# Performance work log

Hardware: AMD Instinct MI355X
Metric: run time of the kernel (lower is better)

Reference implementation:

```python
import jax, jax.numpy as jnp
import numpy as np

L, B, D, Di, N, H, P, K, M, V = 4, 8, 2048, 4096, 128, 64, 64, 4, 8, 50288
Cch = Di + 2 * N           # conv channels = 4352
Dout = 2 * Di + 2 * N + H  # in_proj out = 8512
EPS = 1e-5


def _rms(x, w):
    return x * jax.lax.rsqrt(jnp.mean(x * x, axis=-1, keepdims=True) + EPS) * w


def setup_inputs() -> dict:
    key = jax.random.key(0)
    ks = jax.random.split(key, 16)
    s = 0.02
    return {
        "input_ids": jax.random.randint(ks[0], (B, 1), 0, V),
        "emb": jax.random.normal(ks[1], (V, D)) * s,
        "in_proj_w": jax.random.normal(ks[2], (L, D, Dout)) * s,
        "conv_w": jax.random.normal(ks[3], (L, Cch, K)) * s,
        "conv_b": jax.random.normal(ks[4], (L, Cch)) * s,
        "A_log": jax.random.normal(ks[5], (L, H)) * 0.5,
        "dt_bias": jax.random.normal(ks[6], (L, H)) * 0.5,
        "D_param": jax.random.normal(ks[7], (L, H)) * 0.5,
        "mixer_norm_w": jnp.ones((L, Di)),
        "out_proj_w": jax.random.normal(ks[8], (L, Di, D)) * s,
        "layer_norm_w": jnp.ones((L, D)),
        "norm_f_w": jnp.ones((D,)),
        "W_mc": jax.random.normal(ks[9], (L, M + 1)).at[:, -1].set(5.0),
        "conv_state": jax.random.normal(ks[10], (L, B, Cch, K)) * 0.1,
        "ssm_state": jax.random.normal(ks[11], (L, B, H, P, N)) * 0.1,
        "cached_states": jax.random.normal(ks[12], (L, B, M, H, P, N)) * 0.1,
    }


def reference(input_ids, emb, in_proj_w, conv_w, conv_b, A_log, dt_bias, D_param,
              mixer_norm_w, out_proj_w, layer_norm_w, norm_f_w, W_mc,
              conv_state, ssm_state, cached_states):
    ids = input_ids[:, 0]              # (B,)
    res = emb[ids]                     # (B, D) token embedding gather
    for l in range(L):
        xn = _rms(res, layer_norm_w[l])
        zxbcdt = xn @ in_proj_w[l]     # (B, Dout)
        z = zxbcdt[:, :Di]
        xBC = zxbcdt[:, Di:Di + Cch]
        dt = zxbcdt[:, Di + Cch:]
        # circular conv-state shift + depthwise conv over kernel dim
        cs = jnp.concatenate([conv_state[l][:, :, 1:], xBC[:, :, None]], axis=-1)
        xBC = jax.nn.silu(jnp.sum(cs * conv_w[l][None], axis=-1) + conv_b[l])
        x, Bm, Cm = xBC[:, :Di], xBC[:, Di:Di + N], xBC[:, Di + N:]
        dt = jax.nn.softplus(dt + dt_bias[l])                 # (B, H)
        dA = jnp.exp(dt * (-jnp.exp(A_log[l])))               # (B, H)
        x = x.reshape(B, H, P)
        dBx = jnp.einsum('bh,bn,bhp->bhpn', dt, Bm, x)        # (B,H,P,N)
        ssm = ssm_state[l] * dA[:, :, None, None] + dBx       # (B,H,P,N)
        # softmax-weighted fusion of cached segment states + current state
        w = jax.nn.softmax(W_mc[l])                           # (M+1,)
        fused = jnp.einsum('bmhpn,m->bhpn', cached_states[l], w[:-1]) + w[-1] * ssm
        y = jnp.einsum('bhpn,bn->bhp', fused, Cm) + D_param[l][None, :, None] * x
        y = y.reshape(B, Di)
        y = _rms(y * jax.nn.silu(z), mixer_norm_w[l])         # gated RMSNorm
        res = res + y @ out_proj_w[l]
    res = _rms(res, norm_f_w)
    logits = res @ emb.T               # tied lm_head
    return logits[:, None, :]          # (B, 1, V)
```

## Files before the change

### kernel.cpp

```cpp
#include <hip/hip_runtime.h>
#include <hip/hip_bf16.h>
#include <math.h>

#define LN 4
#define B_ 8
#define D_ 2048
#define DI 4096
#define N_ 128
#define H_ 64
#define P_ 64
#define K_ 4
#define M_ 8
#define V_ 50288
#define CCH (DI + 2*N_)
#define DOUT (2*DI + 2*N_ + H_)
#define EPSF 1e-5f
#define KT_IN 32
#define KT_OUT 128

typedef float f32x4 __attribute__((ext_vector_type(4)));

__device__ inline float wave_sum(float v) {
  #pragma unroll
  for (int off = 32; off > 0; off >>= 1) v += __shfl_xor(v, off, 64);
  return v;
}

__device__ inline float fold_reduce8(const float a[8], int lane) {
  float t0[4];
  #pragma unroll
  for (int r = 0; r < 4; ++r) {
    float keep = (lane & 1) ? a[2*r+1] : a[2*r];
    float send = (lane & 1) ? a[2*r]   : a[2*r+1];
    t0[r] = keep + __shfl_xor(send, 1, 64);
  }
  float t1[2];
  #pragma unroll
  for (int r = 0; r < 2; ++r) {
    float keep = (lane & 2) ? t0[2*r+1] : t0[2*r];
    float send = (lane & 2) ? t0[2*r]   : t0[2*r+1];
    t1[r] = keep + __shfl_xor(send, 2, 64);
  }
  float keep = (lane & 4) ? t1[1] : t1[0];
  float send = (lane & 4) ? t1[0] : t1[1];
  float u = keep + __shfl_xor(send, 4, 64);
  u += __shfl_xor(u, 8, 64);
  u += __shfl_xor(u, 16, 64);
  u += __shfl_xor(u, 32, 64);
  return u;
}

__global__ __launch_bounds__(256)
void k_inproj1_first(const int* __restrict__ ids, const float* __restrict__ emb,
                     const float* __restrict__ lnw, const float* __restrict__ W,
                     float* __restrict__ pin) {
  __shared__ float xs[8][64];
  __shared__ float sred[4][8];
  int tid = threadIdx.x, lane = tid & 63, wid = tid >> 6;
  int jt = blockIdx.x % 9, kt = blockIdx.x / 9;
  int k0 = kt * 64;
  float ssq[8];
  #pragma unroll
  for (int r = 0; r < 8; ++r) {
    const float* row = emb + (size_t)ids[r] * D_;
    f32x4 a = *reinterpret_cast<const f32x4*>(row + tid * 8);
    f32x4 c = *reinterpret_cast<const f32x4*>(row + tid * 8 + 4);
    ssq[r] = a[0]*a[0] + a[1]*a[1] + a[2]*a[2] + a[3]*a[3]
           + c[0]*c[0] + c[1]*c[1] + c[2]*c[2] + c[3]*c[3];
  }
  #pragma unroll
  for (int r = 0; r < 8; ++r) {
    float wsum = wave_sum(ssq[r]);
    if (lane == 0) sred[wid][r] = wsum;
  }
  __syncthreads();
  for (int i = tid; i < 8 * 64; i += 256) {
    int r = i >> 6, kk = i & 63;
    const float* row = emb + (size_t)ids[r] * D_;
    float tot = sred[0][r] + sred[1][r] + sred[2][r] + sred[3][r];
    float scale = rsqrtf(tot / (float)D_ + EPSF);
    xs[r][kk] = row[k0 + kk] * scale * lnw[k0 + kk];
  }
  __syncthreads();
  int j = jt * 1024 + tid * 4;
  if (j >= DOUT) return;
  f32x4 acc[8];
  #pragma unroll
  for (int r = 0; r < 8; ++r) acc[r] = (f32x4)0.f;
  const float* Wp = W + (size_t)k0 * DOUT + j;
  for (int kk = 0; kk < 64; ++kk) {
    f32x4 w4 = __builtin_nontemporal_load(
        reinterpret_cast<const f32x4*>(Wp + (size_t)kk * DOUT));
    #pragma unroll
    for (int r = 0; r < 8; ++r) acc[r] += w4 * xs[r][kk];
  }
  #pragma unroll
  for (int r = 0; r < 8; ++r)
    *reinterpret_cast<f32x4*>(&pin[((size_t)kt * 8 + r) * DOUT + j]) = acc[r];
}

__global__ __launch_bounds__(256)
void k_inproj1(const float* __restrict__ res, const float* __restrict__ ssq_in,
               const float* __restrict__ lnw, const float* __restrict__ W,
               float* __restrict__ pin) {
  __shared__ float xs[8][64];
  int tid = threadIdx.x;
  int jt = blockIdx.x % 9, kt = blockIdx.x / 9;
  int k0 = kt * 64;
  for (int i = tid; i < 8 * 64; i += 256) {
    int r = i >> 6, kk = i & 63;
    float scale = rsqrtf(ssq_in[r] / (float)D_ + EPSF);
    xs[r][kk] = res[r * D_ + k0 + kk] * scale * lnw[k0 + kk];
  }
  __syncthreads();
  int j = jt * 1024 + tid * 4;
  if (j >= DOUT) return;
  f32x4 acc[8];
  #pragma unroll
  for (int r = 0; r < 8; ++r) acc[r] = (f32x4)0.f;
  const float* Wp = W + (size_t)k0 * DOUT + j;
  for (int kk = 0; kk < 64; ++kk) {
    f32x4 w4 = __builtin_nontemporal_load(
        reinterpret_cast<const f32x4*>(Wp + (size_t)kk * DOUT));
    #pragma unroll
    for (int r = 0; r < 8; ++r) acc[r] += w4 * xs[r][kk];
  }
  #pragma unroll
  for (int r = 0; r < 8; ++r)
    *reinterpret_cast<f32x4*>(&pin[((size_t)kt * 8 + r) * DOUT + j]) = acc[r];
}

__global__ __launch_bounds__(256)
void k_inproj2_conv(const float* __restrict__ pin, const float* __restrict__ conv_state,
                    const float* __restrict__ conv_w, const float* __restrict__ conv_b,
                    const float* __restrict__ A_log, const float* __restrict__ dt_bias,
                    const float* __restrict__ W_mc,
                    float* __restrict__ zx, float* __restrict__ xbc,
                    float* __restrict__ dts, float* __restrict__ dav,
                    float* __restrict__ wmc) {
  const int TOT4 = B_ * DOUT / 4;
  int t = blockIdx.x * 256 + threadIdx.x;
  if (t >= TOT4) return;
  f32x4 s = (f32x4)0.f;
  const f32x4* p4 = reinterpret_cast<const f32x4*>(pin) + t;
  #pragma unroll 8
  for (int kt = 0; kt < KT_IN; ++kt) s += p4[(size_t)kt * TOT4];
  reinterpret_cast<f32x4*>(zx)[t] = s;
  int c4 = t * 4;
  int b = c4 / DOUT;
  int c = c4 - b * DOUT;
  #pragma unroll
  for (int e = 0; e < 4; ++e) {
    int ce = c + e;
    if (ce >= DI && ce < DI + CCH) {
      int cc = ce - DI;
      f32x4 cs4 = *reinterpret_cast<const f32x4*>(conv_state + ((size_t)b * CCH + cc) * K_);
      f32x4 cw4 = *reinterpret_cast<const f32x4*>(conv_w + (size_t)cc * K_);
      float v = cs4[1] * cw4[0] + cs4[2] * cw4[1] + cs4[3] * cw4[2]
              + s[e] * cw4[3] + conv_b[cc];
      xbc[b * CCH + cc] = v / (1.f + expf(-v));
    } else if (ce >= DI + CCH) {
      int h = ce - DI - CCH;
      float x = s[e] + dt_bias[h];
      float sp = (x > 20.f) ? x : log1pf(expf(x));
      dts[b * 64 + h] = sp;
      dav[b * 64 + h] = expf(-expf(A_log[h]) * sp);
    }
  }
  if (t == 0) {
    float mx = -1e30f;
    for (int i = 0; i < M_ + 1; ++i) mx = fmaxf(mx, W_mc[i]);
    float e2[M_ + 1], sum = 0.f;
    for (int i = 0; i < M_ + 1; ++i) { e2[i] = expf(W_mc[i] - mx); sum += e2[i]; }
    for (int i = 0; i < M_ + 1; ++i) wmc[i] = e2[i] / sum;
  }
}

__global__ __launch_bounds__(256)
void k_state(const float* __restrict__ xbc, const float* __restrict__ dts,
             const float* __restrict__ dav, const float* __restrict__ Dp_,
             const float* __restrict__ wmc, const float* __restrict__ ssm,
             const float* __restrict__ cached, float* __restrict__ y) {
  int wg = blockIdx.x * 4 + (threadIdx.x >> 6);
  int lane = threadIdx.x & 63;
  int b = wg >> 11;
  int h = (wg >> 5) & 63;
  int pp = wg & 31;
  int hf = lane >> 5, il = lane & 31;
  int p = pp * 2 + hf;
  float xv  = xbc[b * CCH + h * 64 + p];
  float dtv = dts[b * 64 + h];
  float da  = dav[b * 64 + h];
  float w8  = wmc[8];
  const f32x4* xb4 = reinterpret_cast<const f32x4*>(xbc);
  f32x4 B4 = xb4[b * (CCH / 4) + DI / 4 + il];
  f32x4 C4 = xb4[b * (CCH / 4) + DI / 4 + N_ / 4 + il];
  const f32x4* sp4 = reinterpret_cast<const f32x4*>(ssm) +
                     ((size_t)((b * H_ + h) * P_ + p)) * (N_ / 4) + il;
  const f32x4* cp4 = reinterpret_cast<const f32x4*>(cached) +
                     ((size_t)(((b * M_) * H_ + h) * P_ + p)) * (N_ / 4) + il;
  f32x4 s4 = __builtin_nontemporal_load(sp4);
  f32x4 f4 = (s4 * da + B4 * (dtv * xv)) * w8;
  #pragma unroll
  for (int m = 0; m < 8; ++m) {
    f32x4 c4 = __builtin_nontemporal_load(cp4 + (size_t)m * (H_ * P_ * N_ / 4));
    f4 += c4 * wmc[m];
  }
  f4 *= C4;
  float acc = f4[0] + f4[1] + f4[2] + f4[3];
  #pragma unroll
  for (int off = 1; off < 32; off <<= 1) acc += __shfl_xor(acc, off, 64);
  if (il == 0) y[b * DI + h * 64 + p] = acc + Dp_[h] * xv;
}

__global__ void k_gatednorm(const float* __restrict__ y, const float* __restrict__ zx,
                            const float* __restrict__ mnw, float* __restrict__ yg,
                            float* __restrict__ ssq_in) {
  __shared__ float lds[8];
  int b = blockIdx.x;
  if (threadIdx.x == 0) ssq_in[b] = 0.f;
  float tv[16];
  float ss = 0.f;
  #pragma unroll
  for (int t = 0; t < 16; ++t) {
    int i = threadIdx.x + t * 256;
    float z = zx[b * DOUT + i];
    float v = y[b * DI + i] * (z / (1.f + expf(-z)));
    tv[t] = v; ss += v * v;
  }
  float wsum = wave_sum(ss);
  int lane = threadIdx.x & 63, wid = threadIdx.x >> 6;
  if (lane == 0) lds[wid] = wsum;
  __syncthreads();
  float tot = lds[0] + lds[1] + lds[2] + lds[3];
  float scale = rsqrtf(tot / (float)DI + EPSF);
  #pragma unroll
  for (int t = 0; t < 16; ++t) {
    int i = threadIdx.x + t * 256;
    yg[b * DI + i] = tv[t] * scale * mnw[i];
  }
}

__global__ void k_outproj1(const float* __restrict__ yg, const float* __restrict__ W,
                           float* __restrict__ pout) {
  __shared__ float xs[8][32];
  int jt = blockIdx.x & 1, kt = blockIdx.x >> 1;
  int k0 = kt * 32;
  for (int i = threadIdx.x; i < 8 * 32; i += 256) {
    int r = i >> 5, kk = i & 31;
    xs[r][kk] = yg[r * DI + k0 + kk];
  }
  __syncthreads();
  int j = jt * 1024 + threadIdx.x * 4;
  f32x4 acc[8];
  #pragma unroll
  for (int r = 0; r < 8; ++r) acc[r] = (f32x4)0.f;
  const float* Wp = W + (size_t)k0 * D_ + j;
  for (int kk = 0; kk < 32; ++kk) {
    f32x4 w4 = __builtin_nontemporal_load(
        reinterpret_cast<const f32x4*>(Wp + (size_t)kk * D_));
    #pragma unroll
    for (int r = 0; r < 8; ++r) acc[r] += w4 * xs[r][kk];
  }
  #pragma unroll
  for (int r = 0; r < 8; ++r)
    *reinterpret_cast<f32x4*>(&pout[((size_t)kt * 8 + r) * D_ + j]) = acc[r];
}

__global__ __launch_bounds__(256)
void k_outproj2(const float* __restrict__ pout, float* __restrict__ res,
                const int* __restrict__ ids, const float* __restrict__ emb,
                float* __restrict__ ssq_in) {
  __shared__ f32x4 red[256];
  const int TOT4 = B_ * D_ / 4;
  int tid = threadIdx.x;
  int pos = blockIdx.x * 64 + (tid & 63);
  int kq = tid >> 6;
  const f32x4* p4 = reinterpret_cast<const f32x4*>(pout) + pos;
  f32x4 s = (f32x4)0.f;
  #pragma unroll 8
  for (int k = 0; k < 32; ++k)
    s += p4[(size_t)(kq * 32 + k) * TOT4];
  red[tid] = s;
  __syncthreads();
  if (tid < 64) {
    f32x4 tot = red[tid] + red[tid + 64] + red[tid + 128] + red[tid + 192];
    f32x4* r4 = reinterpret_cast<f32x4*>(res);
    f32x4 nv;
    if (ids) {
      int b = pos >> 9, d4 = pos & 511;
      f32x4 base = reinterpret_cast<const f32x4*>(emb)[(size_t)ids[b] * (D_ / 4) + d4];
      nv = base + tot;
    } else {
      nv = r4[pos] + tot;
    }
    r4[pos] = nv;
    float ps = nv[0]*nv[0] + nv[1]*nv[1] + nv[2]*nv[2] + nv[3]*nv[3];
    ps = wave_sum(ps);
    if (tid == 0) atomicAdd(&ssq_in[pos >> 9], ps);
  }
}

#define SL_ 4
#define KS_ (D_ / SL_)
#define NVB16 (V_ / 16)
__global__ __launch_bounds__(256)
void k_logits(const float* __restrict__ res, const float* __restrict__ ssq_in,
              const float* __restrict__ nfw, const float* __restrict__ emb,
              float* __restrict__ pl) {
  __shared__ f32x4 xs[8][KS_ / 4];
  int s = blockIdx.x & 3, vb = blockIdx.x >> 2;
  const f32x4* res4 = reinterpret_cast<const f32x4*>(res);
  const f32x4* nfw4 = reinterpret_cast<const f32x4*>(nfw);
  for (int i = threadIdx.x; i < 8 * (KS_ / 4); i += 256) {
    int r = i >> 7, q = i & 127;
    float scale = rsqrtf(ssq_in[r] / (float)D_ + EPSF);
    xs[r][q] = res4[r * (D_ / 4) + s * (KS_ / 4) + q] * scale
             * nfw4[s * (KS_ / 4) + q];
  }
  __syncthreads();
  int wid = threadIdx.x >> 6, lane = threadIdx.x & 63;
  int v0 = vb * 16 + wid * 4;
  const f32x4* e4 = reinterpret_cast<const f32x4*>(emb);
  #pragma unroll
  for (int vv = 0; vv < 4; ++vv) {
    int v = v0 + vv;
    const f32x4* ep = e4 + (size_t)v * (D_ / 4) + s * (KS_ / 4);
    float acc[8] = {0,0,0,0,0,0,0,0};
    #pragma unroll
    for (int st = 0; st < KS_ / 256; ++st) {
      int c = st * 64 + lane;
      f32x4 e = __builtin_nontemporal_load(ep + c);
      #pragma unroll
      for (int r = 0; r < 8; ++r) {
        f32x4 x = xs[r][c];
        acc[r] += e[0]*x[0] + e[1]*x[1] + e[2]*x[2] + e[3]*x[3];
      }
    }
    float u = fold_reduce8(acc, lane);
    if (lane < 8) pl[((size_t)s * 8 + lane) * V_ + v] = u;
  }
}

__global__ __launch_bounds__(256)
void k_logits2(const float* __restrict__ pl, float* __restrict__ out) {
  int v = blockIdx.x * 256 + threadIdx.x;
  if (v >= V_) return;
  int r = blockIdx.y;
  float t = pl[(size_t)r * V_ + v]
          + pl[((size_t)8  + r) * V_ + v]
          + pl[((size_t)16 + r) * V_ + v]
          + pl[((size_t)24 + r) * V_ + v];
  out[(size_t)r * V_ + v] = t;
}

extern "C" void kernel_launch(void* const* d_in, const int* in_sizes, int n_in,
                              void* d_out, int out_size, void* d_ws, size_t ws_size,
                              hipStream_t stream) {
  const int*   ids    = (const int*)  d_in[0];
  const float* emb    = (const float*)d_in[1];
  const float* inW    = (const float*)d_in[2];
  const float* convW  = (const float*)d_in[3];
  const float* convB  = (const float*)d_in[4];
  const float* Alog   = (const float*)d_in[5];
  const float* dtB    = (const float*)d_in[6];
  const float* Dpar   = (const float*)d_in[7];
  const float* mnw    = (const float*)d_in[8];
  const float* outW   = (const float*)d_in[9];
  const float* lnw    = (const float*)d_in[10];
  const float* nfw    = (const float*)d_in[11];
  const float* Wmc    = (const float*)d_in[12];
  const float* convS  = (const float*)d_in[13];
  const float* ssmS   = (const float*)d_in[14];
  const float* cached = (const float*)d_in[15];
  float* out = (float*)d_out;
  float* ws  = (float*)d_ws;

  float* res   = ws;
  float* zx    = ws + 16384;
  float* xbc   = ws + 84480;
  float* dts   = ws + 119296;
  float* dav   = ws + 119808;
  float* wmc   = ws + 120320;
  float* ssqi  = ws + 120384;
  float* y     = ws + 120448;
  float* yg    = ws + 153216;
  float* pin   = ws + 185984;
  float* pout  = ws + 2365056;
  float* pl    = ws + 4462208;

  for (int l = 0; l < LN; ++l) {
    if (l == 0)
      k_inproj1_first<<<288, 256, 0, stream>>>(ids, emb, lnw,
                                               inW, pin);
    else
      k_inproj1<<<288, 256, 0, stream>>>(res, ssqi, lnw + (size_t)l * D_,
                                         inW + (size_t)l * D_ * DOUT, pin);
    k_inproj2_conv<<<67, 256, 0, stream>>>(pin,
        convS + (size_t)l * B_ * CCH * K_, convW + (size_t)l * CCH * K_,
        convB + (size_t)l * CCH, Alog + l * H_, dtB + l * H_, Wmc + l * (M_ + 1),
        zx, xbc, dts, dav, wmc);
    k_state<<<4096, 256, 0, stream>>>(xbc, dts, dav, Dpar + l * H_, wmc,
        ssmS + (size_t)l * B_ * H_ * P_ * N_,
        cached + (size_t)l * B_ * M_ * H_ * P_ * N_, y);
    k_gatednorm<<<8, 256, 0, stream>>>(y, zx, mnw + (size_t)l * DI, yg, ssqi);
    k_outproj1<<<256, 256, 0, stream>>>(yg, outW + (size_t)l * DI * D_, pout);
    k_outproj2<<<64, 256, 0, stream>>>(pout, res,
                                       (l == 0) ? ids : nullptr, emb, ssqi);
  }
  k_logits<<<NVB16 * SL_, 256, 0, stream>>>(res, ssqi, nfw, emb, pl);
  k_logits2<<<dim3((V_ + 255) / 256, 8), 256, 0, stream>>>(pl, out);
}
```

Baseline: 427.4 us.

## Fuse gated RMSNorm into state and out-proj kernels via atomic sum-of-squares

Removes the separate gated-norm kernel launch, which ran on only 8 blocks. Each state block now computes the squared gated values for its 8 outputs and atomically adds them into a per-batch sum-of-squares buffer. The out-projection kernel applies the SiLU gate, the RMS scale and the norm weight while loading its input tile. The sum buffers are zeroed in the preceding conv kernel. This costs 4096 atomics per layer plus recomputing the gate in every out-projection block, and makes the summation order nondeterministic.

```diff
diff --git a/kernel.cpp b/kernel.cpp
--- a/kernel.cpp
+++ b/kernel.cpp
@@ -137,7 +137,12 @@
                     const float* __restrict__ W_mc,
                     float* __restrict__ zx, float* __restrict__ xbc,
                     float* __restrict__ dts, float* __restrict__ dav,
-                    float* __restrict__ wmc) {
+                    float* __restrict__ wmc, float* __restrict__ ssq_in,
+                    float* __restrict__ gssq) {
+  if (blockIdx.x == 0) {
+    if (threadIdx.x < 8) ssq_in[threadIdx.x] = 0.f;
+    else if (threadIdx.x < 16) gssq[threadIdx.x - 8] = 0.f;
+  }
   const int TOT4 = B_ * DOUT / 4;
   int t = blockIdx.x * 256 + threadIdx.x;
   if (t >= TOT4) return;
@@ -177,10 +182,12 @@
 }
 
 __global__ __launch_bounds__(256)
-void k_state(const float* __restrict__ xbc, const float* __restrict__ dts,
-             const float* __restrict__ dav, const float* __restrict__ Dp_,
-             const float* __restrict__ wmc, const float* __restrict__ ssm,
-             const float* __restrict__ cached, float* __restrict__ y) {
+void k_state(const float* __restrict__ xbc, const float* __restrict__ zx,
+             const float* __restrict__ dts, const float* __restrict__ dav,
+             const float* __restrict__ Dp_, const float* __restrict__ wmc,
+             const float* __restrict__ ssm, const float* __restrict__ cached,
+             float* __restrict__ y, float* __restrict__ gssq) {
+  __shared__ float gred[8];
   int wg = blockIdx.x * 4 + (threadIdx.x >> 6);
   int lane = threadIdx.x & 63;
   int b = wg >> 11;
@@ -210,48 +217,38 @@
   float acc = f4[0] + f4[1] + f4[2] + f4[3];
   #pragma unroll
   for (int off = 1; off < 32; off <<= 1) acc += __shfl_xor(acc, off, 64);
-  if (il == 0) y[b * DI + h * 64 + p] = acc + Dp_[h] * xv;
-}
-
-__global__ void k_gatednorm(const float* __restrict__ y, const float* __restrict__ zx,
-                            const float* __restrict__ mnw, float* __restrict__ yg,
-                            float* __restrict__ ssq_in) {
-  __shared__ float lds[8];
-  int b = blockIdx.x;
-  if (threadIdx.x == 0) ssq_in[b] = 0.f;
-  float tv[16];
-  float ss = 0.f;
-  #pragma unroll
-  for (int t = 0; t < 16; ++t) {
-    int i = threadIdx.x + t * 256;
-    float z = zx[b * DOUT + i];
-    float v = y[b * DI + i] * (z / (1.f + expf(-z)));
-    tv[t] = v; ss += v * v;
-  }
-  float wsum = wave_sum(ss);
-  int lane = threadIdx.x & 63, wid = threadIdx.x >> 6;
-  if (lane == 0) lds[wid] = wsum;
-  __syncthreads();
-  float tot = lds[0] + lds[1] + lds[2] + lds[3];
-  float scale = rsqrtf(tot / (float)DI + EPSF);
-  #pragma unroll
-  for (int t = 0; t < 16; ++t) {
-    int i = threadIdx.x + t * 256;
-    yg[b * DI + i] = tv[t] * scale * mnw[i];
-  }
-}
-
-__global__ void k_outproj1(const float* __restrict__ yg, const float* __restrict__ W,
-                           float* __restrict__ pout) {
+  if (il == 0) {
+    float yv = acc + Dp_[h] * xv;
+    int d = h * 64 + p;
+    y[b * DI + d] = yv;
+    float z = zx[b * DOUT + d];
+    float v = yv * (z / (1.f + expf(-z)));
+    gred[(threadIdx.x >> 6) * 2 + hf] = v * v;
+  }
+  __syncthreads();
+  if (threadIdx.x == 0) {
+    float g = gred[0] + gred[1] + gred[2] + gred[3]
+            + gred[4] + gred[5] + gred[6] + gred[7];
+    atomicAdd(&gssq[b], g);
+  }
+}
+
+__global__ void k_outproj1(const float* __restrict__ y, const float* __restrict__ zx,
+                           const float* __restrict__ mnw, const float* __restrict__ gssq,
+                           const float* __restrict__ W, float* __restrict__ pout) {
   __shared__ float xs[8][32];
+  int tid = threadIdx.x;
   int jt = blockIdx.x & 1, kt = blockIdx.x >> 1;
   int k0 = kt * 32;
-  for (int i = threadIdx.x; i < 8 * 32; i += 256) {
-    int r = i >> 5, kk = i & 31;
-    xs[r][kk] = yg[r * DI + k0 + kk];
-  }
-  __syncthreads();
-  int j = jt * 1024 + threadIdx.x * 4;
+  {
+    int r = tid >> 5, kk = tid & 31;
+    float scale = rsqrtf(gssq[r] / (float)DI + EPSF);
+    float z = zx[r * DOUT + k0 + kk];
+    float g = z / (1.f + expf(-z));
+    xs[r][kk] = y[r * DI + k0 + kk] * g * scale * mnw[k0 + kk];
+  }
+  __syncthreads();
+  int j = jt * 1024 + tid * 4;
   f32x4 acc[8];
   #pragma unroll
   for (int r = 0; r < 8; ++r) acc[r] = (f32x4)0.f;
@@ -383,28 +380,27 @@
   float* dav   = ws + 119808;
   float* wmc   = ws + 120320;
   float* ssqi  = ws + 120384;
-  float* y     = ws + 120448;
-  float* yg    = ws + 153216;
-  float* pin   = ws + 185984;
-  float* pout  = ws + 2365056;
-  float* pl    = ws + 4462208;
+  float* gssq  = ws + 120448;
+  float* y     = ws + 120512;
+  float* pin   = ws + 153280;
+  float* pout  = ws + 2332352;
+  float* pl    = ws + 4429504;
 
   for (int l = 0; l < LN; ++l) {
     if (l == 0)
-      k_inproj1_first<<<288, 256, 0, stream>>>(ids, emb, lnw,
-                                               inW, pin);
+      k_inproj1_first<<<288, 256, 0, stream>>>(ids, emb, lnw, inW, pin);
     else
       k_inproj1<<<288, 256, 0, stream>>>(res, ssqi, lnw + (size_t)l * D_,
                                          inW + (size_t)l * D_ * DOUT, pin);
     k_inproj2_conv<<<67, 256, 0, stream>>>(pin,
         convS + (size_t)l * B_ * CCH * K_, convW + (size_t)l * CCH * K_,
         convB + (size_t)l * CCH, Alog + l * H_, dtB + l * H_, Wmc + l * (M_ + 1),
-        zx, xbc, dts, dav, wmc);
-    k_state<<<4096, 256, 0, stream>>>(xbc, dts, dav, Dpar + l * H_, wmc,
+        zx, xbc, dts, dav, wmc, ssqi, gssq);
+    k_state<<<4096, 256, 0, stream>>>(xbc, zx, dts, dav, Dpar + l * H_, wmc,
         ssmS + (size_t)l * B_ * H_ * P_ * N_,
-        cached + (size_t)l * B_ * M_ * H_ * P_ * N_, y);
-    k_gatednorm<<<8, 256, 0, stream>>>(y, zx, mnw + (size_t)l * DI, yg, ssqi);
-    k_outproj1<<<256, 256, 0, stream>>>(yg, outW + (size_t)l * DI * D_, pout);
+        cached + (size_t)l * B_ * M_ * H_ * P_ * N_, y, gssq);
+    k_outproj1<<<256, 256, 0, stream>>>(y, zx, mnw + (size_t)l * DI, gssq,
+                                        outW + (size_t)l * DI * D_, pout);
     k_outproj2<<<64, 256, 0, stream>>>(pout, res,
                                        (l == 0) ? ids : nullptr, emb, ssqi);
   }
```

Result: slower. 554.8 us (+29.8%).

## Widen split-K reductions, use bigger gated-norm blocks, pad RMS accumulators

Applied to the files above, without the earlier changes.

The split-K reduction kernels for in_proj and out_proj now split the K-partials across several waves and combine them through LDS. This raises grid sizes from 67 to 266 and from 64 to 256 blocks, so more CUs share these small latency-bound steps. The gated-norm kernel goes from 256 to 1024 threads per row. Per-batch sum-of-squares accumulators are padded to a stride of 16 floats to avoid atomic contention and false sharing. The trade-off is an extra LDS round trip and sync per block, plus a small shift in workspace offsets.

```diff
diff --git a/kernel.cpp b/kernel.cpp
--- a/kernel.cpp
+++ b/kernel.cpp
@@ -17,6 +17,7 @@
 #define EPSF 1e-5f
 #define KT_IN 32
 #define KT_OUT 128
+#define SSQS 16
 
 typedef float f32x4 __attribute__((ext_vector_type(4)));
 
@@ -109,7 +110,7 @@
   int k0 = kt * 64;
   for (int i = tid; i < 8 * 64; i += 256) {
     int r = i >> 6, kk = i & 63;
-    float scale = rsqrtf(ssq_in[r] / (float)D_ + EPSF);
+    float scale = rsqrtf(ssq_in[r * SSQS] / (float)D_ + EPSF);
     xs[r][kk] = res[r * D_ + k0 + kk] * scale * lnw[k0 + kk];
   }
   __syncthreads();
@@ -138,36 +139,43 @@
                     float* __restrict__ zx, float* __restrict__ xbc,
                     float* __restrict__ dts, float* __restrict__ dav,
                     float* __restrict__ wmc) {
+  __shared__ f32x4 red[4][64];
   const int TOT4 = B_ * DOUT / 4;
-  int t = blockIdx.x * 256 + threadIdx.x;
-  if (t >= TOT4) return;
+  int tid = threadIdx.x;
+  int el = tid & 63, kq = tid >> 6;
+  int e = blockIdx.x * 64 + el;
   f32x4 s = (f32x4)0.f;
-  const f32x4* p4 = reinterpret_cast<const f32x4*>(pin) + t;
-  #pragma unroll 8
-  for (int kt = 0; kt < KT_IN; ++kt) s += p4[(size_t)kt * TOT4];
-  reinterpret_cast<f32x4*>(zx)[t] = s;
-  int c4 = t * 4;
+  const f32x4* p4 = reinterpret_cast<const f32x4*>(pin) + e;
+  #pragma unroll
+  for (int kk = 0; kk < 8; ++kk)
+    s += p4[(size_t)(kq * 8 + kk) * TOT4];
+  red[kq][el] = s;
+  __syncthreads();
+  if (tid >= 64) return;
+  s = red[0][tid] + red[1][tid] + red[2][tid] + red[3][tid];
+  reinterpret_cast<f32x4*>(zx)[e] = s;
+  int c4 = e * 4;
   int b = c4 / DOUT;
   int c = c4 - b * DOUT;
   #pragma unroll
-  for (int e = 0; e < 4; ++e) {
-    int ce = c + e;
+  for (int q = 0; q < 4; ++q) {
+    int ce = c + q;
     if (ce >= DI && ce < DI + CCH) {
       int cc = ce - DI;
       f32x4 cs4 = *reinterpret_cast<const f32x4*>(conv_state + ((size_t)b * CCH + cc) * K_);
       f32x4 cw4 = *reinterpret_cast<const f32x4*>(conv_w + (size_t)cc * K_);
       float v = cs4[1] * cw4[0] + cs4[2] * cw4[1] + cs4[3] * cw4[2]
-              + s[e] * cw4[3] + conv_b[cc];
+              + s[q] * cw4[3] + conv_b[cc];
       xbc[b * CCH + cc] = v / (1.f + expf(-v));
     } else if (ce >= DI + CCH) {
       int h = ce - DI - CCH;
-      float x = s[e] + dt_bias[h];
+      float x = s[q] + dt_bias[h];
       float sp = (x > 20.f) ? x : log1pf(expf(x));
       dts[b * 64 + h] = sp;
       dav[b * 64 + h] = expf(-expf(A_log[h]) * sp);
     }
   }
-  if (t == 0) {
+  if (blockIdx.x == 0 && tid == 0) {
     float mx = -1e30f;
     for (int i = 0; i < M_ + 1; ++i) mx = fmaxf(mx, W_mc[i]);
     float e2[M_ + 1], sum = 0.f;
@@ -213,30 +221,33 @@
   if (il == 0) y[b * DI + h * 64 + p] = acc + Dp_[h] * xv;
 }
 
-__global__ void k_gatednorm(const float* __restrict__ y, const float* __restrict__ zx,
-                            const float* __restrict__ mnw, float* __restrict__ yg,
-                            float* __restrict__ ssq_in) {
-  __shared__ float lds[8];
-  int b = blockIdx.x;
-  if (threadIdx.x == 0) ssq_in[b] = 0.f;
-  float tv[16];
+__global__ __launch_bounds__(1024)
+void k_gatednorm(const float* __restrict__ y, const float* __restrict__ zx,
+                 const float* __restrict__ mnw, float* __restrict__ yg,
+                 float* __restrict__ ssq_in) {
+  __shared__ float lds[16];
+  int b = blockIdx.x, tid = threadIdx.x;
+  if (tid < 8) ssq_in[tid * SSQS] = 0.f;
+  float tv[4];
   float ss = 0.f;
   #pragma unroll
-  for (int t = 0; t < 16; ++t) {
-    int i = threadIdx.x + t * 256;
+  for (int t = 0; t < 4; ++t) {
+    int i = tid + t * 1024;
     float z = zx[b * DOUT + i];
     float v = y[b * DI + i] * (z / (1.f + expf(-z)));
     tv[t] = v; ss += v * v;
   }
   float wsum = wave_sum(ss);
-  int lane = threadIdx.x & 63, wid = threadIdx.x >> 6;
+  int lane = tid & 63, wid = tid >> 6;
   if (lane == 0) lds[wid] = wsum;
   __syncthreads();
-  float tot = lds[0] + lds[1] + lds[2] + lds[3];
+  float tot = 0.f;
+  #pragma unroll
+  for (int i = 0; i < 16; ++i) tot += lds[i];
   float scale = rsqrtf(tot / (float)DI + EPSF);
   #pragma unroll
-  for (int t = 0; t < 16; ++t) {
-    int i = threadIdx.x + t * 256;
+  for (int t = 0; t < 4; ++t) {
+    int i = tid + t * 1024;
     yg[b * DI + i] = tv[t] * scale * mnw[i];
   }
 }
@@ -271,33 +282,37 @@
 void k_outproj2(const float* __restrict__ pout, float* __restrict__ res,
                 const int* __restrict__ ids, const float* __restrict__ emb,
                 float* __restrict__ ssq_in) {
-  __shared__ f32x4 red[256];
+  __shared__ f32x4 red[16][16];
   const int TOT4 = B_ * D_ / 4;
   int tid = threadIdx.x;
-  int pos = blockIdx.x * 64 + (tid & 63);
-  int kq = tid >> 6;
+  int pl = tid & 15, kq = tid >> 4;
+  int pos = blockIdx.x * 16 + pl;
   const f32x4* p4 = reinterpret_cast<const f32x4*>(pout) + pos;
   f32x4 s = (f32x4)0.f;
-  #pragma unroll 8
-  for (int k = 0; k < 32; ++k)
-    s += p4[(size_t)(kq * 32 + k) * TOT4];
-  red[tid] = s;
-  __syncthreads();
-  if (tid < 64) {
-    f32x4 tot = red[tid] + red[tid + 64] + red[tid + 128] + red[tid + 192];
+  #pragma unroll
+  for (int kk = 0; kk < 8; ++kk)
+    s += p4[(size_t)(kq * 8 + kk) * TOT4];
+  red[pl][kq] = s;
+  __syncthreads();
+  if (tid < 16) {
+    f32x4 tot = (f32x4)0.f;
+    #pragma unroll
+    for (int q = 0; q < 16; ++q) tot += red[tid][q];
+    int mypos = blockIdx.x * 16 + tid;
     f32x4* r4 = reinterpret_cast<f32x4*>(res);
     f32x4 nv;
     if (ids) {
-      int b = pos >> 9, d4 = pos & 511;
+      int b = mypos >> 9, d4 = mypos & 511;
       f32x4 base = reinterpret_cast<const f32x4*>(emb)[(size_t)ids[b] * (D_ / 4) + d4];
       nv = base + tot;
     } else {
-      nv = r4[pos] + tot;
+      nv = r4[mypos] + tot;
     }
-    r4[pos] = nv;
+    r4[mypos] = nv;
     float ps = nv[0]*nv[0] + nv[1]*nv[1] + nv[2]*nv[2] + nv[3]*nv[3];
-    ps = wave_sum(ps);
-    if (tid == 0) atomicAdd(&ssq_in[pos >> 9], ps);
+    #pragma unroll
+    for (int off = 1; off < 16; off <<= 1) ps += __shfl_xor(ps, off, 64);
+    if (tid == 0) atomicAdd(&ssq_in[(mypos >> 9) * SSQS], ps);
   }
 }
 
@@ -314,7 +329,7 @@
   const f32x4* nfw4 = reinterpret_cast<const f32x4*>(nfw);
   for (int i = threadIdx.x; i < 8 * (KS_ / 4); i += 256) {
     int r = i >> 7, q = i & 127;
-    float scale = rsqrtf(ssq_in[r] / (float)D_ + EPSF);
+    float scale = rsqrtf(ssq_in[r * SSQS] / (float)D_ + EPSF);
     xs[r][q] = res4[r * (D_ / 4) + s * (KS_ / 4) + q] * scale
              * nfw4[s * (KS_ / 4) + q];
   }
@@ -383,30 +398,29 @@
   float* dav   = ws + 119808;
   float* wmc   = ws + 120320;
   float* ssqi  = ws + 120384;
-  float* y     = ws + 120448;
-  float* yg    = ws + 153216;
-  float* pin   = ws + 185984;
-  float* pout  = ws + 2365056;
-  float* pl    = ws + 4462208;
+  float* y     = ws + 120512;
+  float* yg    = ws + 153280;
+  float* pin   = ws + 186048;
+  float* pout  = ws + 2365120;
+  float* pl    = ws + 4462272;
 
   for (int l = 0; l < LN; ++l) {
     if (l == 0)
-      k_inproj1_first<<<288, 256, 0, stream>>>(ids, emb, lnw,
-                                               inW, pin);
+      k_inproj1_first<<<288, 256, 0, stream>>>(ids, emb, lnw, inW, pin);
     else
       k_inproj1<<<288, 256, 0, stream>>>(res, ssqi, lnw + (size_t)l * D_,
                                          inW + (size_t)l * D_ * DOUT, pin);
-    k_inproj2_conv<<<67, 256, 0, stream>>>(pin,
+    k_inproj2_conv<<<266, 256, 0, stream>>>(pin,
         convS + (size_t)l * B_ * CCH * K_, convW + (size_t)l * CCH * K_,
         convB + (size_t)l * CCH, Alog + l * H_, dtB + l * H_, Wmc + l * (M_ + 1),
         zx, xbc, dts, dav, wmc);
     k_state<<<4096, 256, 0, stream>>>(xbc, dts, dav, Dpar + l * H_, wmc,
         ssmS + (size_t)l * B_ * H_ * P_ * N_,
         cached + (size_t)l * B_ * M_ * H_ * P_ * N_, y);
-    k_gatednorm<<<8, 256, 0, stream>>>(y, zx, mnw + (size_t)l * DI, yg, ssqi);
+    k_gatednorm<<<8, 1024, 0, stream>>>(y, zx, mnw + (size_t)l * DI, yg, ssqi);
     k_outproj1<<<256, 256, 0, stream>>>(yg, outW + (size_t)l * DI * D_, pout);
-    k_outproj2<<<64, 256, 0, stream>>>(pout, res,
-                                       (l == 0) ? ids : nullptr, emb, ssqi);
+    k_outproj2<<<256, 256, 0, stream>>>(pout, res,
+                                        (l == 0) ? ids : nullptr, emb, ssqi);
   }
   k_logits<<<NVB16 * SL_, 256, 0, stream>>>(res, ssqi, nfw, emb, pl);
   k_logits2<<<dim3((V_ + 255) / 256, 8), 256, 0, stream>>>(pl, out);
```

Result: faster. 418.6 us (-2.1%).
